# Kernel tuning notes

Hardware: AMD Instinct MI355X
Metric: run time of the kernel (lower is better)

Reference implementation:

```python
import jax, jax.numpy as jnp
import numpy as np
from jax import lax

N, C_IN, L, K, C_OUT, PAD = 16, 64, 8192, 3, 64, 1

def setup_inputs() -> dict:
    key = jax.random.key(0)
    k1, k2, k3 = jax.random.split(key, 3)
    x = jax.random.normal(k1, (N, C_IN, L), dtype=jnp.float32)
    # kaiming normal (relu): std = sqrt(2 / fan_in), fan_in = C_in * kernel_size
    std_off = np.sqrt(2.0 / (C_IN * K)).astype(np.float32)
    w_off = jax.random.normal(k2, (2 * K, C_IN, K), dtype=jnp.float32) * std_off
    b_off = jnp.zeros((2 * K,), dtype=jnp.float32)
    # 1x1 conv: fan_in = C_in * K (kernel_size 1)
    std_w = np.sqrt(2.0 / (C_IN * K)).astype(np.float32)
    w = jax.random.normal(k3, (C_OUT, C_IN * K), dtype=jnp.float32) * std_w
    b = jnp.zeros((C_OUT,), dtype=jnp.float32)
    return {"x": x, "w_off": w_off, "b_off": b_off, "w": w, "b": b}

def reference(x, w_off, b_off, w, b):
    n, c, l = x.shape
    # offset conv: Conv1d(C, 2K, K, stride=1, padding=PAD)
    offsets = lax.conv_general_dilated(
        x, w_off, window_strides=(1,), padding=[(PAD, PAD)],
        dimension_numbers=("NCH", "OIH", "NCH")) + b_off[None, :, None]
    l_out = offsets.shape[2]
    # [N, 2K, L] -> [N, K, 2, L] -> [N, L, K, 2]; only component 0 is used
    off = offsets.reshape(n, K, 2, l_out).transpose(0, 3, 1, 2)[..., 0]  # [N, L, K]
    x_pad = jnp.pad(x, ((0, 0), (0, 0), (PAD, PAD)))
    lp = l + 2 * PAD
    base = jnp.arange(PAD, lp - PAD, dtype=x.dtype)[None, :, None]  # [1, L, 1]
    grid = jnp.clip(base + off, 0.0, lp - 1)                        # [N, L, K]
    left = jnp.floor(grid).astype(jnp.int32)
    right = jnp.minimum(left + 1, lp - 1)
    alpha = grid - left.astype(x.dtype)                              # [N, L, K]
    idx_l = left.reshape(n, -1)
    idx_r = right.reshape(n, -1)
    gather = jax.vmap(lambda xp, i: xp[:, i])  # per-sample gather over length axis
    x_left = gather(x_pad, idx_l).reshape(n, c, l_out, K)
    x_right = gather(x_pad, idx_r).reshape(n, c, l_out, K)
    a = alpha[:, None]  # [N, 1, L, K]
    x_deform = (1.0 - a) * x_left + a * x_right                      # [N, C, L, K]
    # replicate torch's permute(0,3,2,1).view(N, C*K, L) exactly (row-major)
    x_deform = x_deform.transpose(0, 3, 2, 1).reshape(n, c * K, l_out)
    out = jnp.einsum("om,nml->nol", w, x_deform) + b[None, :, None]
    return out
```

## Files before the change

### kernel.cpp

```cpp
#include <hip/hip_runtime.h>
#include <hip/hip_bf16.h>
#include <math.h>

#define NB   16
#define CIN  64
#define LEN  8192
#define LP2  8195
#define COUT 64
#define MSZ  192

typedef float    f32x4 __attribute__((ext_vector_type(4)));
typedef _Float16 f16x8 __attribute__((ext_vector_type(8)));
typedef _Float16 f16x2 __attribute__((ext_vector_type(2)));

static __device__ inline unsigned int pkrtz(float lo, float hi) {
    return __builtin_bit_cast(unsigned int, __builtin_amdgcn_cvt_pkrtz(lo, hi));
}

__global__ __launch_bounds__(256) void prep4_kernel(
    const float* __restrict__ x, const float* __restrict__ w_off,
    const float* __restrict__ b_off, const float* __restrict__ w,
    float* __restrict__ gbuf, unsigned int* __restrict__ xt32,
    unsigned short* __restrict__ wtf)
{
    int bid = blockIdx.x;
    int tid = threadIdx.x;

    if (bid >= NB * 128) {
        int b = bid - NB * 128;
        int ot = b / 6, ks = b - ot * 6;
        #pragma unroll
        for (int h = 0; h < 2; ++h) {
            int t2 = tid + h * 256;
            int lq = t2 >> 3, s = t2 & 7;
            int o = ot * 16 + (lq & 15);
            int m = ks * 32 + (lq >> 4) * 8 + s;
            _Float16 hv = (_Float16)w[o * MSZ + m];
            wtf[b * 512 + t2] = __builtin_bit_cast(unsigned short, hv);
        }
        return;
    }

    __shared__ float ps[4][3][64];
    __shared__ unsigned int bt[64 * 33];

    int lane = tid & 63;
    int wid  = __builtin_amdgcn_readfirstlane(tid >> 6);
    int xcd = bid & 7;
    int tt  = bid >> 3;
    int n   = (xcd << 1) | (tt >> 7);
    int t   = tt & 127;
    int l0 = t << 6;
    int l  = l0 + lane;
    const float* xn = x + (size_t)n * (CIN * LEN);
    bool okm = (l >= 1);
    bool okp = (l < LEN - 1);

    float a0 = 0.f, a1 = 0.f, a2 = 0.f;
    unsigned int pk[8];

    #pragma unroll
    for (int ci = 0; ci < 16; ci += 2) {
        int c0 = (wid << 4) | ci;
        const float* xc0 = xn + (size_t)c0 * LEN;
        const float* xc1 = xc0 + LEN;
        float xm0 = okm ? xc0[l - 1] : 0.f;
        float x00 = xc0[l];
        float xp0 = okp ? xc0[l + 1] : 0.f;
        float xm1 = okm ? xc1[l - 1] : 0.f;
        float x01 = xc1[l];
        float xp1 = okp ? xc1[l + 1] : 0.f;
        const float* wa = w_off + (size_t)c0 * 3;
        const float* wb = wa + 384;
        const float* wc = wa + 768;
        a0 = fmaf(wa[0], xm0, a0); a0 = fmaf(wa[1], x00, a0); a0 = fmaf(wa[2], xp0, a0);
        a0 = fmaf(wa[3], xm1, a0); a0 = fmaf(wa[4], x01, a0); a0 = fmaf(wa[5], xp1, a0);
        a1 = fmaf(wb[0], xm0, a1); a1 = fmaf(wb[1], x00, a1); a1 = fmaf(wb[2], xp0, a1);
        a1 = fmaf(wb[3], xm1, a1); a1 = fmaf(wb[4], x01, a1); a1 = fmaf(wb[5], xp1, a1);
        a2 = fmaf(wc[0], xm0, a2); a2 = fmaf(wc[1], x00, a2); a2 = fmaf(wc[2], xp0, a2);
        a2 = fmaf(wc[3], xm1, a2); a2 = fmaf(wc[4], x01, a2); a2 = fmaf(wc[5], xp1, a2);
        pk[ci >> 1] = pkrtz(x00, x01);
    }

    ps[wid][0][lane] = a0;
    ps[wid][1][lane] = a1;
    ps[wid][2][lane] = a2;
    #pragma unroll
    for (int j = 0; j < 8; ++j)
        bt[lane * 33 + (wid << 3) + j] = pk[j];
    __syncthreads();

    if (tid < 192) {
        int k = tid >> 6, ll = tid & 63;
        float s = b_off[2 * k];
        #pragma unroll
        for (int w4 = 0; w4 < 4; ++w4) s += ps[w4][k][ll];
        float g = fminf(fmaxf((float)(l0 + ll + 1) + s, 0.f), 8193.f);
        gbuf[((size_t)n * LEN + l0 + ll) * 3 + k] = g;
    }

    {
        int row = tid >> 2, grp = tid & 3;
        const unsigned int* src = &bt[row * 33 + (grp << 3)];
        uint4 u0, u1;
        u0.x = src[0]; u0.y = src[1]; u0.z = src[2]; u0.w = src[3];
        u1.x = src[4]; u1.y = src[5]; u1.z = src[6]; u1.w = src[7];
        size_t base = ((size_t)n * LP2 + 1 + l0 + row) * 32 + (grp << 3);
        *(uint4*)&xt32[base]     = u0;
        *(uint4*)&xt32[base + 4] = u1;
    }
    if (t == 0   && tid < 32) xt32[((size_t)n * LP2) * 32 + tid] = 0u;
    if (t == 127 && tid < 64) xt32[((size_t)n * LP2 + 8193 + (tid >> 5)) * 32 + (tid & 31)] = 0u;
}

__global__ __launch_bounds__(256) void dconv8_kernel(
    const unsigned short* __restrict__ xt16, const unsigned short* __restrict__ wtf,
    const float* __restrict__ bias, const float* __restrict__ gbuf,
    float* __restrict__ out)
{
    __shared__ unsigned short Bl[MSZ * 64];
    __shared__ __align__(16) int2 meta[MSZ];
    int tid = threadIdx.x;

    int wg  = blockIdx.x;
    int xcd = wg & 7;
    int tt  = wg >> 3;
    int n   = (xcd << 1) | (tt >> 7);
    int p   = tt & 127;

    if (tid < MSZ) {
        int k = tid >> 6, r = tid & 63;
        int l = (r << 7) | p;
        float g  = gbuf[((size_t)n * LEN + l) * 3 + k];
        float fl = floorf(g);
        meta[tid] = make_int2((int)fl, __float_as_int(g - fl));
    }
    __syncthreads();

    const unsigned short* xb = xt16 + (size_t)n * LP2 * 64;

    #pragma unroll
    for (int j = 0; j < 6; ++j) {
        int task = tid + (j << 8);
        int m  = task >> 3;
        int ch = task & 7;
        int2 mv = meta[m];
        float a = __int_as_float(mv.y);
        _Float16 ah = (_Float16)a;
        f16x2 a2; a2[0] = ah; a2[1] = ah;
        const unsigned short* rl = xb + ((size_t)(unsigned)mv.x << 6) + (ch << 3);
        uint4 vl4 = *(const uint4*)rl;
        uint4 vr4 = *(const uint4*)(rl + 64);
        const f16x2* vlh = (const f16x2*)&vl4;
        const f16x2* vrh = (const f16x2*)&vr4;
        uint4 ov;
        unsigned int* ovp = (unsigned int*)&ov;
        #pragma unroll
        for (int q = 0; q < 4; ++q) {
            f16x2 r = vlh[q] + a2 * (vrh[q] - vlh[q]);
            ovp[q] = __builtin_bit_cast(unsigned int, r);
        }
        int dst = (m << 6) + ((ch << 3) ^ (((m >> 3) & 3) << 4));
        *(uint4*)&Bl[dst] = ov;
    }
    __syncthreads();

    int lane = tid & 63;
    int ct   = tid >> 6;
    int g4   = lane >> 4;
    int c    = (ct << 4) | (lane & 15);

    f32x4 acc[4] = {};

    #pragma unroll
    for (int ks = 0; ks < 6; ++ks) {
        int mb = ks * 32 + (g4 << 3);
        int cx = c ^ ((((unsigned)(mb >> 3)) & 3) << 4);
        f16x8 afrag;
        #pragma unroll
        for (int s = 0; s < 8; ++s)
            afrag[s] = __builtin_bit_cast(_Float16, Bl[((mb + s) << 6) + cx]);

        #pragma unroll
        for (int ot = 0; ot < 4; ++ot) {
            f16x8 bfrag = *(const f16x8*)(wtf + ((size_t)(((ot * 6 + ks) << 6) + lane) << 3));
            acc[ot] = __builtin_amdgcn_mfma_f32_16x16x32_f16(afrag, bfrag, acc[ot], 0, 0, 0);
        }
    }

    int q0 = (p << 6) + ct * 16 + g4 * 4;
    #pragma unroll
    for (int ot = 0; ot < 4; ++ot) {
        int o = ot * 16 + (lane & 15);
        float bb = bias[o];
        float4 r4;
        r4.x = acc[ot][0] + bb;
        r4.y = acc[ot][1] + bb;
        r4.z = acc[ot][2] + bb;
        r4.w = acc[ot][3] + bb;
        *(float4*)&out[((size_t)n * COUT + o) * LEN + q0] = r4;
    }
}

extern "C" void kernel_launch(void* const* d_in, const int* in_sizes, int n_in,
                              void* d_out, int out_size, void* d_ws, size_t ws_size,
                              hipStream_t stream) {
    const float* x     = (const float*)d_in[0];
    const float* w_off = (const float*)d_in[1];
    const float* b_off = (const float*)d_in[2];
    const float* w     = (const float*)d_in[3];
    const float* b     = (const float*)d_in[4];
    float* out = (float*)d_out;

    const size_t GBUF_B = (size_t)NB * LEN * 3 * sizeof(float);
    const size_t WTF_B  = (size_t)MSZ * COUT * sizeof(short);
    float*          gbuf = (float*)d_ws;
    unsigned short* wtf  = (unsigned short*)((char*)d_ws + GBUF_B);
    unsigned int*   xt32 = (unsigned int*)((char*)d_ws + GBUF_B + WTF_B);
    unsigned short* xt16 = (unsigned short*)xt32;

    prep4_kernel<<<NB * 128 + 24, 256, 0, stream>>>(x, w_off, b_off, w, gbuf, xt32, wtf);
    dconv8_kernel<<<NB * 128, 256, 0, stream>>>(xt16, wtf, b, gbuf, out);
}
```

Measured before the change: 33.58 us.

## Use 512-thread blocks and compute sample metadata inline in gather

```diff
diff --git a/kernel.cpp b/kernel.cpp
--- a/kernel.cpp
+++ b/kernel.cpp
@@ -113,13 +113,12 @@
     if (t == 127 && tid < 64) xt32[((size_t)n * LP2 + 8193 + (tid >> 5)) * 32 + (tid & 31)] = 0u;
 }
 
-__global__ __launch_bounds__(256) void dconv8_kernel(
+__global__ __launch_bounds__(512) void dconv9_kernel(
     const unsigned short* __restrict__ xt16, const unsigned short* __restrict__ wtf,
     const float* __restrict__ bias, const float* __restrict__ gbuf,
     float* __restrict__ out)
 {
     __shared__ unsigned short Bl[MSZ * 64];
-    __shared__ __align__(16) int2 meta[MSZ];
     int tid = threadIdx.x;
 
     int wg  = blockIdx.x;
@@ -128,27 +127,22 @@
     int n   = (xcd << 1) | (tt >> 7);
     int p   = tt & 127;
 
-    if (tid < MSZ) {
-        int k = tid >> 6, r = tid & 63;
-        int l = (r << 7) | p;
-        float g  = gbuf[((size_t)n * LEN + l) * 3 + k];
-        float fl = floorf(g);
-        meta[tid] = make_int2((int)fl, __float_as_int(g - fl));
-    }
-    __syncthreads();
-
     const unsigned short* xb = xt16 + (size_t)n * LP2 * 64;
-
-    #pragma unroll
-    for (int j = 0; j < 6; ++j) {
-        int task = tid + (j << 8);
+    const float* gb = gbuf + (size_t)n * (LEN * 3);
+
+    #pragma unroll
+    for (int j = 0; j < 3; ++j) {
+        int task = tid + (j << 9);
         int m  = task >> 3;
         int ch = task & 7;
-        int2 mv = meta[m];
-        float a = __int_as_float(mv.y);
-        _Float16 ah = (_Float16)a;
+        int k = m >> 6, r = m & 63;
+        int l = (r << 7) | p;
+        float g  = gb[l * 3 + k];
+        float fl = floorf(g);
+        int   lv = (int)fl;
+        _Float16 ah = (_Float16)(g - fl);
         f16x2 a2; a2[0] = ah; a2[1] = ah;
-        const unsigned short* rl = xb + ((size_t)(unsigned)mv.x << 6) + (ch << 3);
+        const unsigned short* rl = xb + ((size_t)(unsigned)lv << 6) + (ch << 3);
         uint4 vl4 = *(const uint4*)rl;
         uint4 vr4 = *(const uint4*)(rl + 64);
         const f16x2* vlh = (const f16x2*)&vl4;
@@ -157,8 +151,8 @@
         unsigned int* ovp = (unsigned int*)&ov;
         #pragma unroll
         for (int q = 0; q < 4; ++q) {
-            f16x2 r = vlh[q] + a2 * (vrh[q] - vlh[q]);
-            ovp[q] = __builtin_bit_cast(unsigned int, r);
+            f16x2 rr = vlh[q] + a2 * (vrh[q] - vlh[q]);
+            ovp[q] = __builtin_bit_cast(unsigned int, rr);
         }
         int dst = (m << 6) + ((ch << 3) ^ (((m >> 3) & 3) << 4));
         *(uint4*)&Bl[dst] = ov;
@@ -166,11 +160,13 @@
     __syncthreads();
 
     int lane = tid & 63;
-    int ct   = tid >> 6;
+    int wv   = tid >> 6;
+    int ct   = wv & 3;
+    int oh   = wv >> 2;
     int g4   = lane >> 4;
     int c    = (ct << 4) | (lane & 15);
 
-    f32x4 acc[4] = {};
+    f32x4 acc[2] = {};
 
     #pragma unroll
     for (int ks = 0; ks < 6; ++ks) {
@@ -182,22 +178,24 @@
             afrag[s] = __builtin_bit_cast(_Float16, Bl[((mb + s) << 6) + cx]);
 
         #pragma unroll
-        for (int ot = 0; ot < 4; ++ot) {
+        for (int oi = 0; oi < 2; ++oi) {
+            int ot = (oh << 1) | oi;
             f16x8 bfrag = *(const f16x8*)(wtf + ((size_t)(((ot * 6 + ks) << 6) + lane) << 3));
-            acc[ot] = __builtin_amdgcn_mfma_f32_16x16x32_f16(afrag, bfrag, acc[ot], 0, 0, 0);
+            acc[oi] = __builtin_amdgcn_mfma_f32_16x16x32_f16(afrag, bfrag, acc[oi], 0, 0, 0);
         }
     }
 
     int q0 = (p << 6) + ct * 16 + g4 * 4;
     #pragma unroll
-    for (int ot = 0; ot < 4; ++ot) {
-        int o = ot * 16 + (lane & 15);
+    for (int oi = 0; oi < 2; ++oi) {
+        int ot = (oh << 1) | oi;
+        int o  = ot * 16 + (lane & 15);
         float bb = bias[o];
         float4 r4;
-        r4.x = acc[ot][0] + bb;
-        r4.y = acc[ot][1] + bb;
-        r4.z = acc[ot][2] + bb;
-        r4.w = acc[ot][3] + bb;
+        r4.x = acc[oi][0] + bb;
+        r4.y = acc[oi][1] + bb;
+        r4.z = acc[oi][2] + bb;
+        r4.w = acc[oi][3] + bb;
         *(float4*)&out[((size_t)n * COUT + o) * LEN + q0] = r4;
     }
 }
@@ -220,5 +218,5 @@
     unsigned short* xt16 = (unsigned short*)xt32;
 
     prep4_kernel<<<NB * 128 + 24, 256, 0, stream>>>(x, w_off, b_off, w, gbuf, xt32, wtf);
-    dconv8_kernel<<<NB * 128, 256, 0, stream>>>(xt16, wtf, b, gbuf, out);
-}
+    dconv9_kernel<<<NB * 128, 512, 0, stream>>>(xt16, wtf, b, gbuf, out);
+}
```

New measurement: 34.06 us. Within noise of the previous version (+1.4%).
